# Kernel optimization log

Measured on AMD Instinct MI355X. Metric: run time of the kernel, lower is better.

The kernel has to match this reference:

```python
import jax, jax.numpy as jnp
import numpy as np
from jax import lax

S, B, VIN, VOUT, U, E = 64, 256, 128, 128, 1024, 512
START_CODE = 0
T_DEC = 25  # MAX_DECODE_STEPS


def gru_step(x, h, Wih, Whh, bih, bhh):
    # PyTorch GRU cell, gate order r,z,n
    gi = x @ Wih.T + bih
    gh = h @ Whh.T + bhh
    ir, iz, inn = jnp.split(gi, 3, axis=-1)
    hr, hz, hn = jnp.split(gh, 3, axis=-1)
    r = jax.nn.sigmoid(ir + hr)
    z = jax.nn.sigmoid(iz + hz)
    n = jnp.tanh(inn + r * hn)
    return (1.0 - z) * n + z * h


def setup_inputs() -> dict:
    key = jax.random.key(0)
    ks = jax.random.split(key, 20)
    sc = 0.05
    inp = {
        'x': jax.random.normal(ks[0], (S, B, VIN), jnp.float32),
        'x_len': jnp.maximum(jnp.sort(jax.random.randint(ks[1], (B,), 0, S + 1)), 1),
        'enc_Wih': jax.random.normal(ks[2], (3 * U, VIN), jnp.float32) * sc,
        'enc_Whh': jax.random.normal(ks[3], (3 * U, U), jnp.float32) * sc,
        'enc_bih': jnp.zeros((3 * U,), jnp.float32),
        'enc_bhh': jnp.zeros((3 * U,), jnp.float32),
        'dec_Wih': jax.random.normal(ks[4], (3 * U, E + U), jnp.float32) * sc,
        'dec_Whh': jax.random.normal(ks[5], (3 * U, U), jnp.float32) * sc,
        'dec_bih': jnp.zeros((3 * U,), jnp.float32),
        'dec_bhh': jnp.zeros((3 * U,), jnp.float32),
        'o2h_W': jax.random.normal(ks[6], (E, VOUT), jnp.float32) * sc,
        'o2h_b': jnp.zeros((E,), jnp.float32),
        'fc_W': jax.random.normal(ks[7], (VOUT, U), jnp.float32) * sc,
        'fc_b': jnp.zeros((VOUT,), jnp.float32),
        'W1_W': jax.random.normal(ks[8], (U, U), jnp.float32) * sc,
        'W1_b': jnp.zeros((U,), jnp.float32),
        'W2_W': jax.random.normal(ks[9], (U, U), jnp.float32) * sc,
        'W2_b': jnp.zeros((U,), jnp.float32),
        'V_W': jax.random.normal(ks[10], (1, U), jnp.float32) * sc,
        'V_b': jnp.zeros((1,), jnp.float32),
    }
    return inp


def _forward(x, x_len, enc_Wih, enc_Whh, enc_bih, enc_bhh,
             dec_Wih, dec_Whh, dec_bih, dec_bhh,
             o2h_W, o2h_b, fc_W, fc_b, W1_W, W1_b, W2_W, W2_b, V_W, V_b):
    # ---- Encoder GRU with length masking (pack/pad semantics) ----
    h0 = jnp.zeros((B, U), jnp.float32)
    t_idx = jnp.arange(S)

    def enc_step(h, inp_t):
        xt, t = inp_t
        mask = (t < x_len)[:, None]  # [B,1]
        hn = gru_step(xt, h, enc_Wih, enc_Whh, enc_bih, enc_bhh)
        h = jnp.where(mask, hn, h)
        out = jnp.where(mask, hn, 0.0)
        return h, out

    enc_hidden, enc_out = lax.scan(enc_step, h0, (x, t_idx))  # enc_out [S,B,U]
    enc_out = jnp.transpose(enc_out, (1, 0, 2))  # [B,S,U]

    # ---- Greedy decode (teacher_force=False), 25 steps ----
    enc_proj = enc_out @ W1_W.T + W1_b  # precompute W1(enc_output), [B,S,U]
    start = jnp.zeros((B, VOUT), jnp.float32).at[:, START_CODE].set(1.0)

    def dec_step(carry, _):
        h, dec_in = carry
        score = jnp.tanh(enc_proj + (h @ W2_W.T + W2_b)[:, None, :])  # [B,S,U]
        logits = score @ V_W.T + V_b  # [B,S,1]
        attn = jax.nn.softmax(logits, axis=1)
        ctx = jnp.sum(attn * enc_out, axis=1)  # [B,U]
        emb = dec_in @ o2h_W.T + o2h_b  # [B,E]
        gx = jnp.concatenate([ctx, emb], axis=-1)
        hn = gru_step(gx, h, dec_Wih, dec_Whh, dec_bih, dec_bhh)
        pred = hn @ fc_W.T + fc_b  # [B,VOUT]
        onehot = jax.nn.one_hot(jnp.argmax(pred, axis=-1), VOUT, dtype=pred.dtype)
        return (hn, lax.stop_gradient(onehot)), pred

    _, preds = lax.scan(dec_step, (enc_hidden, start), None, length=T_DEC - 1)
    return jnp.concatenate([start[None], preds], axis=0)  # [25,B,VOUT]


def reference(x, x_len, enc_Wih, enc_Whh, enc_bih, enc_bhh,
              dec_Wih, dec_Whh, dec_bih, dec_bhh,
              o2h_W, o2h_b, fc_W, fc_b, W1_W, W1_b, W2_W, W2_b, V_W, V_b):
    return _forward(x, x_len, enc_Wih, enc_Whh, enc_bih, enc_bhh,
                    dec_Wih, dec_Whh, dec_bih, dec_bhh,
                    o2h_W, o2h_b, fc_W, fc_b, W1_W, W1_b, W2_W, W2_b, V_W, V_b)
```

## Files before the change

### kernel.cpp

```cpp
#include <hip/hip_runtime.h>
#include <math.h>

#define SLEN 64
#define BATCH 256
#define VIND 128
#define VOUTD 128
#define UDIM 1024
#define EDIM 512
#define TDEC 25
#define GXW 1536
#define U3 3072
#define NSEG 12

typedef __attribute__((ext_vector_type(8))) short short8;
typedef __attribute__((ext_vector_type(4))) float f32x4;

#define MFMA(acc, A, B) acc = __builtin_amdgcn_mfma_f32_16x16x32_bf16((A), (B), (acc), 0, 0, 0)

__device__ __forceinline__ float sigm(float x) { return 1.f / (1.f + expf(-x)); }

__device__ __forceinline__ float tanhf_fast(float x) {
    float ax = fabsf(x);
    float e = __expf(-2.f * ax);
    float t = (1.f - e) / (1.f + e);
    return copysignf(t, x);
}

__device__ __forceinline__ short f2bf(float f) {
    unsigned u = __float_as_uint(f);
    u += 0x7FFF + ((u >> 16) & 1);
    return (short)(u >> 16);
}
__device__ __forceinline__ float bf2f(short h) {
    return __uint_as_float(((unsigned)(unsigned short)h) << 16);
}

__device__ __forceinline__ size_t pkChunk(int r, int k, int K) {
    return ((size_t)(r >> 4) * (K >> 5) + (k >> 5)) * 64 + ((r & 15) + 16 * ((k >> 3) & 3));
}

union S8 { short s[8]; short8 v; };

__device__ __forceinline__ void writeSplit8(short* Hi, short* Lo, size_t chunk,
                                            const float* vals) {
    S8 h, l;
#pragma unroll
    for (int j = 0; j < 8; j++) {
        short hb = f2bf(vals[j]);
        h.s[j] = hb;
        l.s[j] = f2bf(vals[j] - bf2f(hb));
    }
    ((short8*)Hi)[chunk] = h.v;
    ((short8*)Lo)[chunk] = l.v;
}

__global__ void init_kernel(float* __restrict__ h0, short* __restrict__ hpHi,
                            short* __restrict__ hpLo, float* __restrict__ out0,
                            int* __restrict__ idx,
                            const float* __restrict__ o2h_W,
                            const float* __restrict__ o2h_b,
                            float* __restrict__ o2hT) {
    int i = blockIdx.x * 256 + threadIdx.x;
    if (i < BATCH * UDIM) { h0[i] = 0.f; hpHi[i] = 0; hpLo[i] = 0; }
    if (i < BATCH * VOUTD) out0[i] = ((i & (VOUTD - 1)) == 0) ? 1.f : 0.f;
    if (i < BATCH) idx[i] = 0;
    if (i < VOUTD * EDIM) {
        int v = i >> 9, e = i & (EDIM - 1);
        o2hT[i] = o2h_W[(size_t)e * VOUTD + v] + o2h_b[e];
    }
}

struct PackSeg {
    const float* sA; const float* sB;
    short* Hi; short* Lo;
    int KA, KB, offA, offB, chunkStart;
};
struct PackArgs { PackSeg s[NSEG]; };

__global__ void pack_all(PackArgs pa, int total) {
    int gid = blockIdx.x * 256 + threadIdx.x;
    if (gid >= total) return;
    int si = 0;
#pragma unroll
    for (int i = 1; i < NSEG; i++) si = (gid >= pa.s[i].chunkStart) ? i : si;
    PackSeg sg = pa.s[si];
    int local = gid - sg.chunkStart;
    int K = sg.KA + sg.KB;
    int cpr = K >> 3;
    int r = local / cpr, k0 = (local - r * cpr) * 8;
    const float* src = (k0 < sg.KA)
        ? sg.sA + (size_t)(sg.offA + r) * sg.KA + k0
        : sg.sB + (size_t)(sg.offB + r) * sg.KB + (k0 - sg.KA);
    float v[8];
#pragma unroll
    for (int j = 0; j < 8; j++) v[j] = src[j];
    writeSplit8(sg.Hi, sg.Lo, pkChunk(r, k0, K), v);
}

__global__ __launch_bounds__(256) void gemm_w(
    const short8* __restrict__ Ahi, const short8* __restrict__ Alo,
    const short8* __restrict__ Whi, const short8* __restrict__ Wlo,
    const float* __restrict__ bias, float* __restrict__ C,
    int KT, int N) {
    int tid = threadIdx.x, lane = tid & 63, wave = tid >> 6;
    int m16 = blockIdx.x * 4 + (wave & 1) * 2;
    int nb = blockIdx.y * 8 + (wave >> 1) * 4;
    const short8* a0h = Ahi + (size_t)m16 * KT * 64 + lane;
    const short8* a1h = a0h + (size_t)KT * 64;
    const short8* a0l = Alo + (size_t)m16 * KT * 64 + lane;
    const short8* a1l = a0l + (size_t)KT * 64;
    const short8* w0h = Whi + (size_t)(nb + 0) * KT * 64 + lane;
    const short8* w1h = Whi + (size_t)(nb + 1) * KT * 64 + lane;
    const short8* w2h = Whi + (size_t)(nb + 2) * KT * 64 + lane;
    const short8* w3h = Whi + (size_t)(nb + 3) * KT * 64 + lane;
    const short8* w0l = Wlo + (size_t)(nb + 0) * KT * 64 + lane;
    const short8* w1l = Wlo + (size_t)(nb + 1) * KT * 64 + lane;
    const short8* w2l = Wlo + (size_t)(nb + 2) * KT * 64 + lane;
    const short8* w3l = Wlo + (size_t)(nb + 3) * KT * 64 + lane;
    f32x4 acc0[4] = {}, acc1[4] = {};

    for (int kt = 0; kt < KT; kt++) {
        size_t o = (size_t)kt * 64;
        short8 A0H = a0h[o], A1H = a1h[o], A0L = a0l[o], A1L = a1l[o];
        short8 WH0 = w0h[o], WL0 = w0l[o];
        MFMA(acc0[0], A0H, WH0); MFMA(acc1[0], A1H, WH0);
        MFMA(acc0[0], A0H, WL0); MFMA(acc1[0], A1H, WL0);
        MFMA(acc0[0], A0L, WH0); MFMA(acc1[0], A1L, WH0);
        short8 WH1 = w1h[o], WL1 = w1l[o];
        MFMA(acc0[1], A0H, WH1); MFMA(acc1[1], A1H, WH1);
        MFMA(acc0[1], A0H, WL1); MFMA(acc1[1], A1H, WL1);
        MFMA(acc0[1], A0L, WH1); MFMA(acc1[1], A1L, WH1);
        short8 WH2 = w2h[o], WL2 = w2l[o];
        MFMA(acc0[2], A0H, WH2); MFMA(acc1[2], A1H, WH2);
        MFMA(acc0[2], A0H, WL2); MFMA(acc1[2], A1H, WL2);
        MFMA(acc0[2], A0L, WH2); MFMA(acc1[2], A1L, WH2);
        short8 WH3 = w3h[o], WL3 = w3l[o];
        MFMA(acc0[3], A0H, WH3); MFMA(acc1[3], A1H, WH3);
        MFMA(acc0[3], A0H, WL3); MFMA(acc1[3], A1H, WL3);
        MFMA(acc0[3], A0L, WH3); MFMA(acc1[3], A1L, WH3);
    }
    int rsub = (lane >> 4) * 4, cn = lane & 15;
    int row0 = (m16 + 0) * 16 + rsub;
    int row1 = (m16 + 1) * 16 + rsub;
#pragma unroll
    for (int j = 0; j < 4; j++) {
        int col = (nb + j) * 16 + cn;
        float bb = bias ? bias[col] : 0.f;
#pragma unroll
        for (int r = 0; r < 4; r++) {
            C[(size_t)(row0 + r) * N + col] = acc0[j][r] + bb;
            C[(size_t)(row1 + r) * N + col] = acc1[j][r] + bb;
        }
    }
}

__global__ __launch_bounds__(256) void gemm_bm32(
    const short8* __restrict__ Ahi, const short8* __restrict__ Alo,
    const short8* __restrict__ Whi, const short8* __restrict__ Wlo,
    const float* __restrict__ bias, float* __restrict__ C,
    int KT, int N) {
    int tid = threadIdx.x, lane = tid & 63, wave = tid >> 6;
    int m16 = blockIdx.x * 2 + (wave & 1);
    int n16 = blockIdx.y * 4 + (wave >> 1) * 2;
    const short8* ah = Ahi + (size_t)m16 * KT * 64 + lane;
    const short8* al = Alo + (size_t)m16 * KT * 64 + lane;
    const short8* w0h = Whi + (size_t)n16 * KT * 64 + lane;
    const short8* w1h = w0h + (size_t)KT * 64;
    const short8* w0l = Wlo + (size_t)n16 * KT * 64 + lane;
    const short8* w1l = w0l + (size_t)KT * 64;
    f32x4 a0 = {0,0,0,0}, a1 = {0,0,0,0};
    for (int kt = 0; kt < KT; kt++) {
        size_t o = (size_t)kt * 64;
        short8 AH = ah[o], AL = al[o];
        short8 W0H = w0h[o], W0L = w0l[o], W1H = w1h[o], W1L = w1l[o];
        MFMA(a0, AH, W0H); MFMA(a1, AH, W1H);
        MFMA(a0, AH, W0L); MFMA(a1, AH, W1L);
        MFMA(a0, AL, W0H); MFMA(a1, AL, W1H);
    }
    int rsub = (lane >> 4) * 4, cn = lane & 15;
    float b0 = bias ? bias[(n16 + 0) * 16 + cn] : 0.f;
    float b1 = bias ? bias[(n16 + 1) * 16 + cn] : 0.f;
#pragma unroll
    for (int r = 0; r < 4; r++) {
        int row = m16 * 16 + rsub + r;
        C[(size_t)row * N + (n16 + 0) * 16 + cn] = a0[r] + b0;
        C[(size_t)row * N + (n16 + 1) * 16 + cn] = a1[r] + b1;
    }
}

__global__ __launch_bounds__(768) void enc_gru3(
    const short8* __restrict__ hinH8, const short8* __restrict__ hinL8,
    const short8* __restrict__ WrH, const short8* __restrict__ WrL,
    const short8* __restrict__ WzH, const short8* __restrict__ WzL,
    const short8* __restrict__ WnH, const short8* __restrict__ WnL,
    const float* __restrict__ gi,
    const float* __restrict__ bih, const float* __restrict__ bhh,
    const float* __restrict__ hinF, float* __restrict__ houtF,
    short* __restrict__ hoH, short* __restrict__ hoL,
    short* __restrict__ eaHi, short* __restrict__ eaLo,
    const int* __restrict__ x_len, int t) {
    __shared__ float sC[6][4][16][16];
    __shared__ float sHo[4][16][16];
    __shared__ float sEo[4][16][16];
    int tid = threadIdx.x, lane = tid & 63, wave = tid >> 6;
    int g = blockIdx.x;
    int m16a = blockIdx.y * 4;
    int gate = wave >> 2, hm = wave & 3, half = hm >> 1, mp = hm & 1;
    int t0 = mp * 2;
    const short8* a0h = hinH8 + (size_t)(m16a + t0) * 32 * 64 + (size_t)half * 16 * 64 + lane;
    const short8* a0l = hinL8 + (size_t)(m16a + t0) * 32 * 64 + (size_t)half * 16 * 64 + lane;
    const short8* a1h = a0h + (size_t)32 * 64;
    const short8* a1l = a0l + (size_t)32 * 64;
    const short8* WH0 = (gate == 0) ? WrH : (gate == 1) ? WzH : WnH;
    const short8* WL0 = (gate == 0) ? WrL : (gate == 1) ? WzL : WnL;
    const short8* wh = WH0 + (size_t)g * 32 * 64 + (size_t)half * 16 * 64 + lane;
    const short8* wl = WL0 + (size_t)g * 32 * 64 + (size_t)half * 16 * 64 + lane;
    f32x4 acc0 = {0, 0, 0, 0}, acc1 = {0, 0, 0, 0};
    for (int kt = 0; kt < 16; kt++) {
        size_t o = (size_t)kt * 64;
        short8 WH = wh[o], WL = wl[o];
        short8 A0H = a0h[o], A0L = a0l[o];
        MFMA(acc0, A0H, WH); MFMA(acc0, A0H, WL); MFMA(acc0, A0L, WH);
        short8 A1H = a1h[o], A1L = a1l[o];
        MFMA(acc1, A1H, WH); MFMA(acc1, A1H, WL); MFMA(acc1, A1L, WH);
    }
    {
        int slot = gate * 2 + half;
        int rsub = (lane >> 4) << 2, cn = lane & 15;
#pragma unroll
        for (int j = 0; j < 4; j++) {
            sC[slot][t0 + 0][rsub + j][cn] = acc0[j];
            sC[slot][t0 + 1][rsub + j][cn] = acc1[j];
        }
    }
    __syncthreads();
    if (wave < 4) {
        int tile = wave;
        int m16 = m16a + tile;
        int cu = g * 16 + (lane & 15);
        int rsub = (lane >> 4) << 2;
        float b_r = bih[cu] + bhh[cu];
        float b_z = bih[UDIM + cu] + bhh[UDIM + cu];
        float b_nh = bhh[2 * UDIM + cu];
        float b_ni = bih[2 * UDIM + cu];
        int growLocal = (t & 15) * 256;
#pragma unroll
        for (int j = 0; j < 4; j++) {
            int rr = rsub + j, cc = lane & 15;
            int b = m16 * 16 + rr;
            const float* gr = gi + (size_t)(growLocal + b) * U3;
            float rg = sigm(sC[0][tile][rr][cc] + sC[1][tile][rr][cc] + gr[cu] + b_r);
            float zg = sigm(sC[2][tile][rr][cc] + sC[3][tile][rr][cc] + gr[UDIM + cu] + b_z);
            float nn = tanhf(gr[2 * UDIM + cu] + b_ni +
                             rg * (sC[4][tile][rr][cc] + sC[5][tile][rr][cc] + b_nh));
            float hp = hinF[(size_t)b * UDIM + cu];
            float hv = (1.f - zg) * nn + zg * hp;
            bool msk = t < x_len[b];
            float ho = msk ? hv : hp;
            houtF[(size_t)b * UDIM + cu] = ho;
            sHo[tile][rr][cc] = ho;
            sEo[tile][rr][cc] = msk ? hv : 0.f;
        }
    }
    __syncthreads();
    if (wave >= 4 && wave < 8 && lane < 32) {
        int tile = wave - 4;
        int m16 = m16a + tile;
        int rr = lane >> 1, oct = lane & 1;
        int brow = m16 * 16 + rr;
        int u0 = g * 16 + oct * 8;
        float v[8];
#pragma unroll
        for (int j = 0; j < 8; j++) v[j] = sHo[tile][rr][oct * 8 + j];
        writeSplit8(hoH, hoL, pkChunk(brow, u0, UDIM), v);
#pragma unroll
        for (int j = 0; j < 8; j++) v[j] = sEo[tile][rr][oct * 8 + j];
        writeSplit8(eaHi, eaLo, pkChunk(brow * SLEN + t, u0, UDIM), v);
    }
}

__global__ __launch_bounds__(768) void dec_gru3(
    const short8* __restrict__ hinH8, const short8* __restrict__ hinL8,
    const short8* __restrict__ gxH8, const short8* __restrict__ gxL8,
    const short8* __restrict__ WrH, const short8* __restrict__ WrL,
    const short8* __restrict__ WzH, const short8* __restrict__ WzL,
    const short8* __restrict__ WnhH, const short8* __restrict__ WnhL,
    const short8* __restrict__ WniH, const short8* __restrict__ WniL,
    const float* __restrict__ bih, const float* __restrict__ bhh,
    const float* __restrict__ hinF, float* __restrict__ houtF,
    short* __restrict__ hoH, short* __restrict__ hoL) {
    __shared__ float sC[8][4][16][16];
    __shared__ float sHo[4][16][16];
    int tid = threadIdx.x, lane = tid & 63, wave = tid >> 6;
    int g = blockIdx.x;
    int m16a = blockIdx.y * 4;
    int gate = wave >> 2, hm = wave & 3, half = hm >> 1, mp = hm & 1;
    int t0 = mp * 2;
    const short8* a0h = hinH8 + (size_t)(m16a + t0) * 32 * 64 + (size_t)half * 16 * 64 + lane;
    const short8* a0l = hinL8 + (size_t)(m16a + t0) * 32 * 64 + (size_t)half * 16 * 64 + lane;
    const short8* a1h = a0h + (size_t)32 * 64;
    const short8* a1l = a0l + (size_t)32 * 64;
    const short8* g0h = gxH8 + (size_t)(m16a + t0) * 48 * 64 + (size_t)half * 24 * 64 + lane;
    const short8* g0l = gxL8 + (size_t)(m16a + t0) * 48 * 64 + (size_t)half * 24 * 64 + lane;
    const short8* g1h = g0h + (size_t)48 * 64;
    const short8* g1l = g0l + (size_t)48 * 64;
    const short8 *whA, *wlA, *whB, *wlB;
    if (gate == 0) {
        whA = WrH + (size_t)g * 80 * 64 + (size_t)half * 16 * 64 + lane;
        wlA = WrL + (size_t)g * 80 * 64 + (size_t)half * 16 * 64 + lane;
        whB = WrH + (size_t)g * 80 * 64 + (size_t)(32 + half * 24) * 64 + lane;
        wlB = WrL + (size_t)g * 80 * 64 + (size_t)(32 + half * 24) * 64 + lane;
    } else if (gate == 1) {
        whA = WzH + (size_t)g * 80 * 64 + (size_t)half * 16 * 64 + lane;
        wlA = WzL + (size_t)g * 80 * 64 + (size_t)half * 16 * 64 + lane;
        whB = WzH + (size_t)g * 80 * 64 + (size_t)(32 + half * 24) * 64 + lane;
        wlB = WzL + (size_t)g * 80 * 64 + (size_t)(32 + half * 24) * 64 + lane;
    } else {
        whA = WnhH + (size_t)g * 32 * 64 + (size_t)half * 16 * 64 + lane;
        wlA = WnhL + (size_t)g * 32 * 64 + (size_t)half * 16 * 64 + lane;
        whB = WniH + (size_t)g * 48 * 64 + (size_t)half * 24 * 64 + lane;
        wlB = WniL + (size_t)g * 48 * 64 + (size_t)half * 24 * 64 + lane;
    }
    f32x4 accA0 = {0,0,0,0}, accA1 = {0,0,0,0};
    f32x4 accB0 = {0,0,0,0}, accB1 = {0,0,0,0};
    for (int kt = 0; kt < 16; kt++) {
        size_t o = (size_t)kt * 64;
        short8 WH = whA[o], WL = wlA[o];
        short8 A0H = a0h[o], A0L = a0l[o];
        MFMA(accA0, A0H, WH); MFMA(accA0, A0H, WL); MFMA(accA0, A0L, WH);
        short8 A1H = a1h[o], A1L = a1l[o];
        MFMA(accA1, A1H, WH); MFMA(accA1, A1H, WL); MFMA(accA1, A1L, WH);
    }
    for (int kt = 0; kt < 24; kt++) {
        size_t o = (size_t)kt * 64;
        short8 WH = whB[o], WL = wlB[o];
        short8 G0H = g0h[o], G0L = g0l[o];
        MFMA(accB0, G0H, WH); MFMA(accB0, G0H, WL); MFMA(accB0, G0L, WH);
        short8 G1H = g1h[o], G1L = g1l[o];
        MFMA(accB1, G1H, WH); MFMA(accB1, G1H, WL); MFMA(accB1, G1L, WH);
    }
    {
        int rsub = (lane >> 4) << 2, cn = lane & 15;
        if (gate < 2) {
            int slot = gate * 2 + half;
#pragma unroll
            for (int j = 0; j < 4; j++) {
                sC[slot][t0 + 0][rsub + j][cn] = accA0[j] + accB0[j];
                sC[slot][t0 + 1][rsub + j][cn] = accA1[j] + accB1[j];
            }
        } else {
#pragma unroll
            for (int j = 0; j < 4; j++) {
                sC[4 + half][t0 + 0][rsub + j][cn] = accA0[j];
                sC[4 + half][t0 + 1][rsub + j][cn] = accA1[j];
                sC[6 + half][t0 + 0][rsub + j][cn] = accB0[j];
                sC[6 + half][t0 + 1][rsub + j][cn] = accB1[j];
            }
        }
    }
    __syncthreads();
    if (wave < 4) {
        int tile = wave;
        int m16 = m16a + tile;
        int cu = g * 16 + (lane & 15);
        int rsub = (lane >> 4) << 2;
        float b_r = bih[cu] + bhh[cu];
        float b_z = bih[UDIM + cu] + bhh[UDIM + cu];
        float b_nh = bhh[2 * UDIM + cu];
        float b_ni = bih[2 * UDIM + cu];
#pragma unroll
        for (int j = 0; j < 4; j++) {
            int rr = rsub + j, cc = lane & 15;
            int b = m16 * 16 + rr;
            float rg = sigm(sC[0][tile][rr][cc] + sC[1][tile][rr][cc] + b_r);
            float zg = sigm(sC[2][tile][rr][cc] + sC[3][tile][rr][cc] + b_z);
            float nn = tanhf(sC[6][tile][rr][cc] + sC[7][tile][rr][cc] + b_ni +
                             rg * (sC[4][tile][rr][cc] + sC[5][tile][rr][cc] + b_nh));
            float hp = hinF[(size_t)b * UDIM + cu];
            float hv = (1.f - zg) * nn + zg * hp;
            houtF[(size_t)b * UDIM + cu] = hv;
            sHo[tile][rr][cc] = hv;
        }
    }
    __syncthreads();
    if (wave >= 4 && wave < 8 && lane < 32) {
        int tile = wave - 4;
        int m16 = m16a + tile;
        int rr = lane >> 1, oct = lane & 1;
        int brow = m16 * 16 + rr;
        int u0 = g * 16 + oct * 8;
        float v[8];
#pragma unroll
        for (int j = 0; j < 8; j++) v[j] = sHo[tile][rr][oct * 8 + j];
        writeSplit8(hoH, hoL, pkChunk(brow, u0, UDIM), v);
    }
}

__global__ __launch_bounds__(1024) void attn_ctx(
    const float* __restrict__ encProj,
    const short* __restrict__ eaHi, const short* __restrict__ eaLo,
    const float* __restrict__ tmp2, const float* __restrict__ V_W,
    const float* __restrict__ V_b,
    const float* __restrict__ o2hT,
    const int* __restrict__ idx, short* __restrict__ gxHi, short* __restrict__ gxLo) {
    int b = blockIdx.x;
    int tid = threadIdx.x, lane = tid & 63, wave = tid >> 6;
    __shared__ float s_t2[UDIM];
    __shared__ float s_v[UDIM];
    __shared__ float s_attn[SLEN];
    __shared__ float s_part[7][128][9];
    for (int u = tid; u < UDIM; u += 1024) {
        s_t2[u] = tmp2[(size_t)b * UDIM + u];
        s_v[u] = V_W[u];
    }
    __syncthreads();
    for (int s = wave; s < SLEN; s += 16) {
        const float4* ep4 = (const float4*)(encProj + ((size_t)b * SLEN + s) * UDIM);
        float p = 0.f;
        for (int u4 = lane; u4 < UDIM / 4; u4 += 64) {
            float4 e = ep4[u4];
            int u = 4 * u4;
            p += tanhf_fast(e.x + s_t2[u]) * s_v[u] +
                 tanhf_fast(e.y + s_t2[u + 1]) * s_v[u + 1] +
                 tanhf_fast(e.z + s_t2[u + 2]) * s_v[u + 2] +
                 tanhf_fast(e.w + s_t2[u + 3]) * s_v[u + 3];
        }
#pragma unroll
        for (int off = 32; off > 0; off >>= 1) p += __shfl_xor(p, off);
        if (lane == 0) s_attn[s] = p + V_b[0];
    }
    __syncthreads();
    if (tid < 64) {
        float v = s_attn[tid];
        float mx = v;
#pragma unroll
        for (int off = 32; off > 0; off >>= 1) mx = fmaxf(mx, __shfl_xor(mx, off));
        float e = expf(v - mx);
        float sum = e;
#pragma unroll
        for (int off = 32; off > 0; off >>= 1) sum += __shfl_xor(sum, off);
        s_attn[tid] = e / sum;
    }
    __syncthreads();
    {
        int grp = tid >> 7, tu = tid & 127;
        int u0 = tu * 8;
        float a[8] = {0, 0, 0, 0, 0, 0, 0, 0};
        const short8* hi8 = (const short8*)eaHi;
        const short8* lo8 = (const short8*)eaLo;
        int lanePart = 16 * ((u0 >> 3) & 3);
        int colPart = u0 >> 5;
        for (int s = grp * 8; s < grp * 8 + 8; s++) {
            int r = b * SLEN + s;
            size_t ch = ((size_t)(r >> 4) * (UDIM >> 5) + colPart) * 64 + (r & 15) + lanePart;
            S8 h, l;
            h.v = hi8[ch];
            l.v = lo8[ch];
            float w = s_attn[s];
#pragma unroll
            for (int j = 0; j < 8; j++) a[j] += w * (bf2f(h.s[j]) + bf2f(l.s[j]));
        }
        if (grp) {
#pragma unroll
            for (int j = 0; j < 8; j++) s_part[grp - 1][tu][j] = a[j];
        }
        __syncthreads();
        if (tid < 128) {
#pragma unroll
            for (int gg = 0; gg < 7; gg++)
#pragma unroll
                for (int j = 0; j < 8; j++) a[j] += s_part[gg][tu][j];
            writeSplit8(gxHi, gxLo, pkChunk(b, u0, GXW), a);
        } else if (tid < 192) {
            int e0 = (tid - 128) * 8;
            int ib = idx[b];
            const float* row = o2hT + (size_t)ib * EDIM + e0;
            float v[8];
#pragma unroll
            for (int j = 0; j < 8; j++) v[j] = row[j];
            writeSplit8(gxHi, gxLo, pkChunk(b, UDIM + e0, GXW), v);
        }
    }
}

__global__ __launch_bounds__(256) void fcw2(
    const short8* __restrict__ hHi, const short8* __restrict__ hLo,
    const short8* __restrict__ fcH, const short8* __restrict__ fcL,
    const float* __restrict__ fc_b, float* __restrict__ pred,
    int* __restrict__ idx,
    const short8* __restrict__ w2H, const short8* __restrict__ w2L,
    const float* __restrict__ W2_b, float* __restrict__ tmp2) {
    __shared__ float sP[16][129];
    int tid = threadIdx.x, lane = tid & 63, wave = tid >> 6;
    if (blockIdx.x < 16) {
        int fm = blockIdx.x;
        const short8* ah = hHi + (size_t)fm * 32 * 64 + lane;
        const short8* al = hLo + (size_t)fm * 32 * 64 + lane;
        int n0 = 2 * wave, n1 = 2 * wave + 1;
        const short8* w0h = fcH + (size_t)n0 * 32 * 64 + lane;
        const short8* w0l = fcL + (size_t)n0 * 32 * 64 + lane;
        const short8* w1h = fcH + (size_t)n1 * 32 * 64 + lane;
        const short8* w1l = fcL + (size_t)n1 * 32 * 64 + lane;
        f32x4 a0 = {0,0,0,0}, a1 = {0,0,0,0};
        for (int kt = 0; kt < 32; kt++) {
            size_t o = (size_t)kt * 64;
            short8 AH = ah[o], AL = al[o];
            short8 W0H = w0h[o], W0L = w0l[o], W1H = w1h[o], W1L = w1l[o];
            MFMA(a0, AH, W0H); MFMA(a1, AH, W1H);
            MFMA(a0, AH, W0L); MFMA(a1, AH, W1L);
            MFMA(a0, AL, W0H); MFMA(a1, AL, W1H);
        }
        int cn = lane & 15, rsub = (lane >> 4) << 2;
#pragma unroll
        for (int j = 0; j < 4; j++) {
            sP[rsub + j][n0 * 16 + cn] = a0[j] + fc_b[n0 * 16 + cn];
            sP[rsub + j][n1 * 16 + cn] = a1[j] + fc_b[n1 * 16 + cn];
        }
        __syncthreads();
        {
            int row = tid >> 4, c0 = (tid & 15) * 8;
            float* pr = pred + (size_t)(fm * 16 + row) * VOUTD;
#pragma unroll
            for (int j = 0; j < 8; j++) pr[c0 + j] = sP[row][c0 + j];
        }
        if (tid < 128) {
            int row = tid >> 3, seg = tid & 7;
            float v = -1e30f;
            int bi = 0;
            int c0 = seg * 16;
            for (int j = c0; j < c0 + 16; j++) {
                float w = sP[row][j];
                if (w > v) { v = w; bi = j; }
            }
#pragma unroll
            for (int off = 1; off < 8; off <<= 1) {
                float ov = __shfl_xor(v, off);
                int obi = __shfl_xor(bi, off);
                if (ov > v || (ov == v && obi < bi)) { v = ov; bi = obi; }
            }
            if (seg == 0) idx[fm * 16 + row] = bi;
        }
    } else {
        int lin = blockIdx.x - 16;
        int bx = lin & 7, by = lin >> 3;
        int m16 = bx * 2 + (wave & 1);
        int n16 = by * 4 + (wave >> 1) * 2;
        const short8* ah = hHi + (size_t)m16 * 32 * 64 + lane;
        const short8* al = hLo + (size_t)m16 * 32 * 64 + lane;
        const short8* w0h = w2H + (size_t)n16 * 32 * 64 + lane;
        const short8* w1h = w0h + (size_t)32 * 64;
        const short8* w0l = w2L + (size_t)n16 * 32 * 64 + lane;
        const short8* w1l = w0l + (size_t)32 * 64;
        f32x4 a0 = {0,0,0,0}, a1 = {0,0,0,0};
        for (int kt = 0; kt < 32; kt++) {
            size_t o = (size_t)kt * 64;
            short8 AH = ah[o], AL = al[o];
            short8 W0H = w0h[o], W0L = w0l[o], W1H = w1h[o], W1L = w1l[o];
            MFMA(a0, AH, W0H); MFMA(a1, AH, W1H);
            MFMA(a0, AH, W0L); MFMA(a1, AH, W1L);
            MFMA(a0, AL, W0H); MFMA(a1, AL, W1H);
        }
        int rsub = (lane >> 4) * 4, cn = lane & 15;
        float b0 = W2_b[(n16 + 0) * 16 + cn];
        float b1 = W2_b[(n16 + 1) * 16 + cn];
#pragma unroll
        for (int r = 0; r < 4; r++) {
            int row = m16 * 16 + rsub + r;
            tmp2[(size_t)row * UDIM + (n16 + 0) * 16 + cn] = a0[r] + b0;
            tmp2[(size_t)row * UDIM + (n16 + 1) * 16 + cn] = a1[r] + b1;
        }
    }
}

extern "C" void kernel_launch(void* const* d_in, const int* in_sizes, int n_in,
                              void* d_out, int out_size, void* d_ws, size_t ws_size,
                              hipStream_t stream) {
    const float* x       = (const float*)d_in[0];
    const int*   x_len   = (const int*)d_in[1];
    const float* enc_Wih = (const float*)d_in[2];
    const float* enc_Whh = (const float*)d_in[3];
    const float* enc_bih = (const float*)d_in[4];
    const float* enc_bhh = (const float*)d_in[5];
    const float* dec_Wih = (const float*)d_in[6];
    const float* dec_Whh = (const float*)d_in[7];
    const float* dec_bih = (const float*)d_in[8];
    const float* dec_bhh = (const float*)d_in[9];
    const float* o2h_W   = (const float*)d_in[10];
    const float* o2h_b   = (const float*)d_in[11];
    const float* fc_W    = (const float*)d_in[12];
    const float* fc_b    = (const float*)d_in[13];
    const float* W1_W    = (const float*)d_in[14];
    const float* W1_b    = (const float*)d_in[15];
    const float* W2_W    = (const float*)d_in[16];
    const float* W2_b    = (const float*)d_in[17];
    const float* V_W     = (const float*)d_in[18];
    const float* V_b     = (const float*)d_in[19];
    float* out = (float*)d_out;

    char* p = (char*)d_ws;
    auto alloc = [&](size_t bytes) -> char* {
        char* q = p;
        p += (bytes + 255) & ~(size_t)255;
        return q;
    };
    float* hAF  = (float*)alloc((size_t)BATCH * UDIM * 4);
    float* hBF  = (float*)alloc((size_t)BATCH * UDIM * 4);
    short* hAH  = (short*)alloc((size_t)BATCH * UDIM * 2);
    short* hAL  = (short*)alloc((size_t)BATCH * UDIM * 2);
    short* hBH  = (short*)alloc((size_t)BATCH * UDIM * 2);
    short* hBL  = (short*)alloc((size_t)BATCH * UDIM * 2);
    float* tmp2 = (float*)alloc((size_t)BATCH * UDIM * 4);
    short* gxHi = (short*)alloc((size_t)BATCH * GXW * 2);
    short* gxLo = (short*)alloc((size_t)BATCH * GXW * 2);
    short* encAHi = (short*)alloc((size_t)BATCH * SLEN * UDIM * 2);
    short* encALo = (short*)alloc((size_t)BATCH * SLEN * UDIM * 2);
    float* encProjF = (float*)alloc((size_t)BATCH * SLEN * UDIM * 4);
    float* gihBuf = encProjF;
    short* eWihH = (short*)alloc((size_t)U3 * VIND * 2);
    short* eWihL = (short*)alloc((size_t)U3 * VIND * 2);
    short* eWrH = (short*)alloc((size_t)UDIM * UDIM * 2);
    short* eWrL = (short*)alloc((size_t)UDIM * UDIM * 2);
    short* eWzH = (short*)alloc((size_t)UDIM * UDIM * 2);
    short* eWzL = (short*)alloc((size_t)UDIM * UDIM * 2);
    short* eWnH = (short*)alloc((size_t)UDIM * UDIM * 2);
    short* eWnL = (short*)alloc((size_t)UDIM * UDIM * 2);
    short* dWrH = (short*)alloc((size_t)UDIM * 2560 * 2);
    short* dWrL = (short*)alloc((size_t)UDIM * 2560 * 2);
    short* dWzH = (short*)alloc((size_t)UDIM * 2560 * 2);
    short* dWzL = (short*)alloc((size_t)UDIM * 2560 * 2);
    short* dWnhH = (short*)alloc((size_t)UDIM * UDIM * 2);
    short* dWnhL = (short*)alloc((size_t)UDIM * UDIM * 2);
    short* dWniH = (short*)alloc((size_t)UDIM * GXW * 2);
    short* dWniL = (short*)alloc((size_t)UDIM * GXW * 2);
    short* w1Hi = (short*)alloc((size_t)UDIM * UDIM * 2);
    short* w1Lo = (short*)alloc((size_t)UDIM * UDIM * 2);
    short* w2Hi = (short*)alloc((size_t)UDIM * UDIM * 2);
    short* w2Lo = (short*)alloc((size_t)UDIM * UDIM * 2);
    short* fcHi = (short*)alloc((size_t)VOUTD * UDIM * 2);
    short* fcLo = (short*)alloc((size_t)VOUTD * UDIM * 2);
    short* xHi  = (short*)alloc((size_t)SLEN * BATCH * VIND * 2);
    short* xLo  = (short*)alloc((size_t)SLEN * BATCH * VIND * 2);
    int*   idx  = (int*)alloc(BATCH * 4);
    float* o2hT = (float*)alloc((size_t)VOUTD * EDIM * 4);

    init_kernel<<<(BATCH * UDIM + 255) / 256, 256, 0, stream>>>(
        hAF, hAH, hAL, out, idx, o2h_W, o2h_b, o2hT);

    {
        PackArgs pa;
        int cs = 0, n = 0;
        auto seg = [&](const float* sA, int KA, int offA, const float* sB, int KB,
                       int offB, short* Hi, short* Lo, int R) {
            pa.s[n] = {sA, sB, Hi, Lo, KA, KB, offA, offB, cs};
            cs += R * (KA + KB) / 8;
            n++;
        };
        seg(enc_Wih, VIND, 0, nullptr, 0, 0, eWihH, eWihL, U3);
        seg(enc_Whh, UDIM, 0, nullptr, 0, 0, eWrH, eWrL, UDIM);
        seg(enc_Whh, UDIM, UDIM, nullptr, 0, 0, eWzH, eWzL, UDIM);
        seg(enc_Whh, UDIM, 2 * UDIM, nullptr, 0, 0, eWnH, eWnL, UDIM);
        seg(dec_Whh, UDIM, 0, dec_Wih, GXW, 0, dWrH, dWrL, UDIM);
        seg(dec_Whh, UDIM, UDIM, dec_Wih, GXW, UDIM, dWzH, dWzL, UDIM);
        seg(dec_Whh, UDIM, 2 * UDIM, nullptr, 0, 0, dWnhH, dWnhL, UDIM);
        seg(dec_Wih, GXW, 2 * UDIM, nullptr, 0, 0, dWniH, dWniL, UDIM);
        seg(W1_W, UDIM, 0, nullptr, 0, 0, w1Hi, w1Lo, UDIM);
        seg(W2_W, UDIM, 0, nullptr, 0, 0, w2Hi, w2Lo, UDIM);
        seg(fc_W, UDIM, 0, nullptr, 0, 0, fcHi, fcLo, VOUTD);
        seg(x, VIND, 0, nullptr, 0, 0, xHi, xLo, SLEN * BATCH);
        pack_all<<<(cs + 255) / 256, 256, 0, stream>>>(pa, cs);
    }

    float* hcF = hAF; float* hnF = hBF;
    short *hcH = hAH, *hcL = hAL, *hnH = hBH, *hnL = hBL;
    for (int c = 0; c < 4; c++) {
        gemm_w<<<dim3(64, 24), 256, 0, stream>>>(
            (const short8*)xHi + (size_t)c * 256 * 4 * 64,
            (const short8*)xLo + (size_t)c * 256 * 4 * 64,
            (const short8*)eWihH, (const short8*)eWihL,
            nullptr, gihBuf, VIND / 32, U3);
        for (int tt = 0; tt < 16; tt++) {
            int t = c * 16 + tt;
            enc_gru3<<<dim3(64, 4), 768, 0, stream>>>(
                (const short8*)hcH, (const short8*)hcL,
                (const short8*)eWrH, (const short8*)eWrL,
                (const short8*)eWzH, (const short8*)eWzL,
                (const short8*)eWnH, (const short8*)eWnL,
                gihBuf, enc_bih, enc_bhh, hcF, hnF, hnH, hnL,
                encAHi, encALo, x_len, t);
            { float* tf = hcF; hcF = hnF; hnF = tf; }
            { short* th = hcH; hcH = hnH; hnH = th; th = hcL; hcL = hnL; hnL = th; }
        }
    }

    gemm_w<<<dim3(SLEN * BATCH / 64, UDIM / 128), 256, 0, stream>>>(
        (const short8*)encAHi, (const short8*)encALo,
        (const short8*)w1Hi, (const short8*)w1Lo,
        W1_b, encProjF, UDIM / 32, UDIM);

    gemm_bm32<<<dim3(BATCH / 32, UDIM / 64), 256, 0, stream>>>(
        (const short8*)hcH, (const short8*)hcL,
        (const short8*)w2Hi, (const short8*)w2Lo,
        W2_b, tmp2, UDIM / 32, UDIM);

    for (int st = 0; st < TDEC - 1; st++) {
        attn_ctx<<<BATCH, 1024, 0, stream>>>(
            encProjF, encAHi, encALo, tmp2, V_W, V_b, o2hT, idx, gxHi, gxLo);
        dec_gru3<<<dim3(64, 4), 768, 0, stream>>>(
            (const short8*)hcH, (const short8*)hcL,
            (const short8*)gxHi, (const short8*)gxLo,
            (const short8*)dWrH, (const short8*)dWrL,
            (const short8*)dWzH, (const short8*)dWzL,
            (const short8*)dWnhH, (const short8*)dWnhL,
            (const short8*)dWniH, (const short8*)dWniL,
            dec_bih, dec_bhh, hcF, hnF, hnH, hnL);
        float* pred = out + (size_t)(1 + st) * BATCH * VOUTD;
        int nblk = (st == TDEC - 2) ? 16 : 144;
        fcw2<<<nblk, 256, 0, stream>>>(
            (const short8*)hnH, (const short8*)hnL,
            (const short8*)fcHi, (const short8*)fcLo,
            fc_b, pred, idx,
            (const short8*)w2Hi, (const short8*)w2Lo, W2_b, tmp2);
        { float* tf = hcF; hcF = hnF; hnF = tf; }
        { short* th = hcH; hcH = hnH; hnH = th; th = hcL; hcL = hnL; hnL = th; }
    }
}
```

Before: 3.443 ms.

## Fuse encoder input projection into per-step GRU kernel

Drops the chunked input-projection GEMM launches and their fp32 gate buffer. Each encoder GRU step now computes x_t·Wih inside the recurrent kernel with split-bf16 MFMAs. The r and z input terms go straight into the hidden accumulators, and the n-gate input term gets its own accumulators and shared-memory slots. This removes four launches and the global round-trip of a large fp32 buffer, but adds a small amount of MFMA work to every one of the 64 serial steps.

```diff
diff --git a/kernel.cpp b/kernel.cpp
--- a/kernel.cpp
+++ b/kernel.cpp
@@ -190,16 +190,17 @@
 
 __global__ __launch_bounds__(768) void enc_gru3(
     const short8* __restrict__ hinH8, const short8* __restrict__ hinL8,
+    const short8* __restrict__ xH8, const short8* __restrict__ xL8,
+    const short8* __restrict__ WihH, const short8* __restrict__ WihL,
     const short8* __restrict__ WrH, const short8* __restrict__ WrL,
     const short8* __restrict__ WzH, const short8* __restrict__ WzL,
     const short8* __restrict__ WnH, const short8* __restrict__ WnL,
-    const float* __restrict__ gi,
     const float* __restrict__ bih, const float* __restrict__ bhh,
     const float* __restrict__ hinF, float* __restrict__ houtF,
     short* __restrict__ hoH, short* __restrict__ hoL,
     short* __restrict__ eaHi, short* __restrict__ eaLo,
     const int* __restrict__ x_len, int t) {
-    __shared__ float sC[6][4][16][16];
+    __shared__ float sC[8][4][16][16];
     __shared__ float sHo[4][16][16];
     __shared__ float sEo[4][16][16];
     int tid = threadIdx.x, lane = tid & 63, wave = tid >> 6;
@@ -215,22 +216,61 @@
     const short8* WL0 = (gate == 0) ? WrL : (gate == 1) ? WzL : WnL;
     const short8* wh = WH0 + (size_t)g * 32 * 64 + (size_t)half * 16 * 64 + lane;
     const short8* wl = WL0 + (size_t)g * 32 * 64 + (size_t)half * 16 * 64 + lane;
-    f32x4 acc0 = {0, 0, 0, 0}, acc1 = {0, 0, 0, 0};
+    const short8* x0h = xH8 + ((size_t)(t * 16 + m16a + t0) * 4 + half * 2) * 64 + lane;
+    const short8* x0l = xL8 + ((size_t)(t * 16 + m16a + t0) * 4 + half * 2) * 64 + lane;
+    const short8* x1h = x0h + (size_t)4 * 64;
+    const short8* x1l = x0l + (size_t)4 * 64;
+    const short8* wxh = WihH + ((size_t)(gate * 64 + g) * 4 + half * 2) * 64 + lane;
+    const short8* wxl = WihL + ((size_t)(gate * 64 + g) * 4 + half * 2) * 64 + lane;
+
+    f32x4 accA0 = {0, 0, 0, 0}, accA1 = {0, 0, 0, 0};
     for (int kt = 0; kt < 16; kt++) {
         size_t o = (size_t)kt * 64;
         short8 WH = wh[o], WL = wl[o];
         short8 A0H = a0h[o], A0L = a0l[o];
-        MFMA(acc0, A0H, WH); MFMA(acc0, A0H, WL); MFMA(acc0, A0L, WH);
+        MFMA(accA0, A0H, WH); MFMA(accA0, A0H, WL); MFMA(accA0, A0L, WH);
         short8 A1H = a1h[o], A1L = a1l[o];
-        MFMA(acc1, A1H, WH); MFMA(acc1, A1H, WL); MFMA(acc1, A1L, WH);
+        MFMA(accA1, A1H, WH); MFMA(accA1, A1H, WL); MFMA(accA1, A1L, WH);
+    }
+    f32x4 accX0 = {0, 0, 0, 0}, accX1 = {0, 0, 0, 0};
+    if (gate < 2) {
+#pragma unroll
+        for (int kt = 0; kt < 2; kt++) {
+            size_t o = (size_t)kt * 64;
+            short8 WH = wxh[o], WL = wxl[o];
+            short8 X0H = x0h[o], X0L = x0l[o];
+            MFMA(accA0, X0H, WH); MFMA(accA0, X0H, WL); MFMA(accA0, X0L, WH);
+            short8 X1H = x1h[o], X1L = x1l[o];
+            MFMA(accA1, X1H, WH); MFMA(accA1, X1H, WL); MFMA(accA1, X1L, WH);
+        }
+    } else {
+#pragma unroll
+        for (int kt = 0; kt < 2; kt++) {
+            size_t o = (size_t)kt * 64;
+            short8 WH = wxh[o], WL = wxl[o];
+            short8 X0H = x0h[o], X0L = x0l[o];
+            MFMA(accX0, X0H, WH); MFMA(accX0, X0H, WL); MFMA(accX0, X0L, WH);
+            short8 X1H = x1h[o], X1L = x1l[o];
+            MFMA(accX1, X1H, WH); MFMA(accX1, X1H, WL); MFMA(accX1, X1L, WH);
+        }
     }
     {
-        int slot = gate * 2 + half;
         int rsub = (lane >> 4) << 2, cn = lane & 15;
-#pragma unroll
-        for (int j = 0; j < 4; j++) {
-            sC[slot][t0 + 0][rsub + j][cn] = acc0[j];
-            sC[slot][t0 + 1][rsub + j][cn] = acc1[j];
+        if (gate < 2) {
+            int slot = gate * 2 + half;
+#pragma unroll
+            for (int j = 0; j < 4; j++) {
+                sC[slot][t0 + 0][rsub + j][cn] = accA0[j];
+                sC[slot][t0 + 1][rsub + j][cn] = accA1[j];
+            }
+        } else {
+#pragma unroll
+            for (int j = 0; j < 4; j++) {
+                sC[4 + half][t0 + 0][rsub + j][cn] = accA0[j];
+                sC[4 + half][t0 + 1][rsub + j][cn] = accA1[j];
+                sC[6 + half][t0 + 0][rsub + j][cn] = accX0[j];
+                sC[6 + half][t0 + 1][rsub + j][cn] = accX1[j];
+            }
         }
     }
     __syncthreads();
@@ -243,16 +283,17 @@
         float b_z = bih[UDIM + cu] + bhh[UDIM + cu];
         float b_nh = bhh[2 * UDIM + cu];
         float b_ni = bih[2 * UDIM + cu];
-        int growLocal = (t & 15) * 256;
 #pragma unroll
         for (int j = 0; j < 4; j++) {
             int rr = rsub + j, cc = lane & 15;
             int b = m16 * 16 + rr;
-            const float* gr = gi + (size_t)(growLocal + b) * U3;
-            float rg = sigm(sC[0][tile][rr][cc] + sC[1][tile][rr][cc] + gr[cu] + b_r);
-            float zg = sigm(sC[2][tile][rr][cc] + sC[3][tile][rr][cc] + gr[UDIM + cu] + b_z);
-            float nn = tanhf(gr[2 * UDIM + cu] + b_ni +
-                             rg * (sC[4][tile][rr][cc] + sC[5][tile][rr][cc] + b_nh));
+            float rS = sC[0][tile][rr][cc] + sC[1][tile][rr][cc];
+            float zS = sC[2][tile][rr][cc] + sC[3][tile][rr][cc];
+            float nhS = sC[4][tile][rr][cc] + sC[5][tile][rr][cc];
+            float niS = sC[6][tile][rr][cc] + sC[7][tile][rr][cc];
+            float rg = sigm(rS + b_r);
+            float zg = sigm(zS + b_z);
+            float nn = tanhf(niS + b_ni + rg * (nhS + b_nh));
             float hp = hinF[(size_t)b * UDIM + cu];
             float hv = (1.f - zg) * nn + zg * hp;
             bool msk = t < x_len[b];
@@ -615,7 +656,6 @@
     short* encAHi = (short*)alloc((size_t)BATCH * SLEN * UDIM * 2);
     short* encALo = (short*)alloc((size_t)BATCH * SLEN * UDIM * 2);
     float* encProjF = (float*)alloc((size_t)BATCH * SLEN * UDIM * 4);
-    float* gihBuf = encProjF;
     short* eWihH = (short*)alloc((size_t)U3 * VIND * 2);
     short* eWihL = (short*)alloc((size_t)U3 * VIND * 2);
     short* eWrH = (short*)alloc((size_t)UDIM * UDIM * 2);
@@ -672,24 +712,18 @@
 
     float* hcF = hAF; float* hnF = hBF;
     short *hcH = hAH, *hcL = hAL, *hnH = hBH, *hnL = hBL;
-    for (int c = 0; c < 4; c++) {
-        gemm_w<<<dim3(64, 24), 256, 0, stream>>>(
-            (const short8*)xHi + (size_t)c * 256 * 4 * 64,
-            (const short8*)xLo + (size_t)c * 256 * 4 * 64,
+    for (int t = 0; t < SLEN; t++) {
+        enc_gru3<<<dim3(64, 4), 768, 0, stream>>>(
+            (const short8*)hcH, (const short8*)hcL,
+            (const short8*)xHi, (const short8*)xLo,
             (const short8*)eWihH, (const short8*)eWihL,
-            nullptr, gihBuf, VIND / 32, U3);
-        for (int tt = 0; tt < 16; tt++) {
-            int t = c * 16 + tt;
-            enc_gru3<<<dim3(64, 4), 768, 0, stream>>>(
-                (const short8*)hcH, (const short8*)hcL,
-                (const short8*)eWrH, (const short8*)eWrL,
-                (const short8*)eWzH, (const short8*)eWzL,
-                (const short8*)eWnH, (const short8*)eWnL,
-                gihBuf, enc_bih, enc_bhh, hcF, hnF, hnH, hnL,
-                encAHi, encALo, x_len, t);
-            { float* tf = hcF; hcF = hnF; hnF = tf; }
-            { short* th = hcH; hcH = hnH; hnH = th; th = hcL; hcL = hnL; hnL = th; }
-        }
+            (const short8*)eWrH, (const short8*)eWrL,
+            (const short8*)eWzH, (const short8*)eWzL,
+            (const short8*)eWnH, (const short8*)eWnL,
+            enc_bih, enc_bhh, hcF, hnF, hnH, hnL,
+            encAHi, encALo, x_len, t);
+        { float* tf = hcF; hcF = hnF; hnF = tf; }
+        { short* th = hcH; hcH = hnH; hnH = th; th = hcL; hcL = hnL; hnL = th; }
     }
 
     gemm_w<<<dim3(SLEN * BATCH / 64, UDIM / 128), 256, 0, stream>>>(
```

New measurement: 3.352 ms (median of 2 runs). -2.6%, faster.
